# Optimization experiments

Hardware: AMD Instinct MI355X
Metric: run time of the kernel (lower is better)

The kernel has to match this reference:

```python
import jax, jax.numpy as jnp
import numpy as np

NEG_INF = -9e15
ALPHA = 0.2  # leaky relu slope


def setup_inputs() -> dict:
    key = jax.random.key(0)
    k1, k2, k3, k4 = jax.random.split(key, 4)
    B, N, Din = 8, 1024, 128
    H, D = 8, 16
    h = jax.random.normal(k1, (B, N, Din), dtype=jnp.float32)
    adj = jax.random.randint(k2, (B, N, N), 0, 2, dtype=jnp.int32)
    W = jax.random.normal(k3, (Din, H * D), dtype=jnp.float32) * 0.1
    a = jax.random.normal(k4, (H, 2 * D, 1), dtype=jnp.float32) * 0.1
    return {"h": h, "adj": adj, "W": W, "a": a}


def reference(h, adj, W, a):
    B, N, _ = h.shape
    H, twoD, _ = a.shape
    D = twoD // 2
    # Wh: [B, N, H, D]
    Wh = (h @ W).reshape(B, N, H, D)
    # Decompose additive attention: a . [Wh_i ; Wh_j] = a_src . Wh_i + a_dst . Wh_j
    a_src = a[:, :D, 0]   # [H, D]
    a_dst = a[:, D:, 0]   # [H, D]
    s_i = jnp.einsum('bnhd,hd->bhn', Wh, a_src)  # [B, H, N]
    s_j = jnp.einsum('bnhd,hd->bhn', Wh, a_dst)  # [B, H, N]
    scores = jax.nn.leaky_relu(s_i[:, :, :, None] + s_j[:, :, None, :], ALPHA)  # [B,H,N,N]
    scores = jnp.where(adj[:, None, :, :] == 0, NEG_INF, scores)
    attn = jax.nn.softmax(scores, axis=-1)  # [B, H, N, N]
    # Weighted aggregation over neighbors j
    h_prime = jnp.einsum('bhij,bjhd->bihd', attn, Wh).reshape(B, N, H * D)
    return h_prime
```

## Files before the change

kernel.cpp:

```cpp
#include <hip/hip_runtime.h>
#include <hip/hip_bf16.h>

constexpr int B   = 8;
constexpr int N   = 1024;
constexpr int DIN = 128;
constexpr int H   = 8;
constexpr int D   = 16;
constexpr int HD  = 128;
constexpr int TI  = 16;
constexpr int TJ  = 128;
constexpr int NT  = N / TJ;

#define LOG2E 1.4426950408889634f
#define TCLAMP 30.0f

typedef __attribute__((ext_vector_type(8))) short bf16x8;
typedef __attribute__((ext_vector_type(4))) float f32x4;

__device__ inline float fast_exp2(float x) {
#if __has_builtin(__builtin_amdgcn_exp2f)
    return __builtin_amdgcn_exp2f(x);
#else
    return exp2f(x);
#endif
}

__global__ __launch_bounds__(256) void k_proj(
    const float* __restrict__ hsrc,
    const float* __restrict__ W,
    const float* __restrict__ a,
    __hip_bfloat16* __restrict__ WhT,
    float* __restrict__ tI,
    float* __restrict__ tJ)
{
    const int blk  = blockIdx.x;
    const int row0 = blk * 64;
    const int b    = row0 >> 10;
    const int n0   = row0 & (N - 1);
    const int t    = threadIdx.x;
    const int lane = t & 63, wave = t >> 6;
    const int mn   = lane & 15, kg = lane >> 4;

    __shared__ __align__(16) __hip_bfloat16 hA[64][136];
    __shared__ __align__(16) __hip_bfloat16 Wt[128][136];

    {
        const float4* hf = reinterpret_cast<const float4*>(hsrc + (size_t)row0 * DIN);
        #pragma unroll
        for (int u = 0; u < 8; ++u) {
            const int idx = t + u * 256;
            const float4 v = hf[idx];
            const int r = idx >> 5, c4 = (idx & 31) * 4;
            __hip_bfloat162 p0, p1;
            p0.x = __float2bfloat16(v.x); p0.y = __float2bfloat16(v.y);
            p1.x = __float2bfloat16(v.z); p1.y = __float2bfloat16(v.w);
            *reinterpret_cast<__hip_bfloat162*>(&hA[r][c4])     = p0;
            *reinterpret_cast<__hip_bfloat162*>(&hA[r][c4 + 2]) = p1;
        }
    }
    {
        const float4* wf = reinterpret_cast<const float4*>(W);
        #pragma unroll
        for (int u = 0; u < 16; ++u) {
            const int idx = t + u * 256;
            const float4 v = wf[idx];
            const int k = idx >> 5, c0 = (idx & 31) * 4;
            Wt[c0][k]     = __float2bfloat16(v.x);
            Wt[c0 + 1][k] = __float2bfloat16(v.y);
            Wt[c0 + 2][k] = __float2bfloat16(v.z);
            Wt[c0 + 3][k] = __float2bfloat16(v.w);
        }
    }
    __syncthreads();

    const int lr0 = wave * 16;
    f32x4 acc[8];
    #pragma unroll
    for (int f = 0; f < 8; ++f) acc[f] = (f32x4){0.f, 0.f, 0.f, 0.f};

    #pragma unroll
    for (int kk = 0; kk < 4; ++kk) {
        const bf16x8 af = *reinterpret_cast<const bf16x8*>(
            &hA[lr0 + mn][kk * 32 + kg * 8]);
        #pragma unroll
        for (int f = 0; f < 8; ++f) {
            const bf16x8 bf = *reinterpret_cast<const bf16x8*>(
                &Wt[f * 16 + mn][kk * 32 + kg * 8]);
            acc[f] = __builtin_amdgcn_mfma_f32_16x16x32_bf16(af, bf, acc[f], 0, 0, 0);
        }
    }

    #pragma unroll
    for (int f = 0; f < 8; ++f) {
        const float as = a[f * 32 + mn];
        const float ad = a[f * 32 + 16 + mn];
        #pragma unroll
        for (int r = 0; r < 4; ++r) {
            const int n = n0 + lr0 + kg * 4 + r;
            WhT[((size_t)(b * HD + f * 16 + mn)) * N + n] = __float2bfloat16(acc[f][r]);
            float vi = acc[f][r] * as;
            float vj = acc[f][r] * ad;
            #pragma unroll
            for (int m = 1; m < 16; m <<= 1) {
                vi += __shfl_xor(vi, m);
                vj += __shfl_xor(vj, m);
            }
            if (mn == 0) {
                tI[((size_t)(b * H + f)) * N + n] = fminf(vi * LOG2E, TCLAMP);
                tJ[((size_t)(b * H + f)) * N + n] = fminf(vj * LOG2E, TCLAMP);
            }
        }
    }
}

__global__ __launch_bounds__(512, 4) void k_attn(
    const int*            __restrict__ adj,
    const __hip_bfloat16* __restrict__ WhT,
    const float*          __restrict__ tI,
    const float*          __restrict__ tJ,
    float*                __restrict__ out)
{
    const int b    = blockIdx.y;
    const int i0   = blockIdx.x * TI;
    const int t    = threadIdx.x;
    const int lane = t & 63, wave = t >> 6;
    const int mn   = lane & 15, kg = lane >> 4;
    const int jp   = lane;
    const int ig2  = wave;

    __shared__ __align__(16) __hip_bfloat16 pl[2][H][TI][136];

    float A[2][8];
    #pragma unroll
    for (int ii = 0; ii < 2; ++ii)
        #pragma unroll
        for (int h = 0; h < 8; ++h)
            A[ii][h] = tI[((size_t)(b * H + h)) * N + i0 + 2 * ig2 + ii];

    f32x4 accO = {0.f, 0.f, 0.f, 0.f};
    f32x4 accD = {0.f, 0.f, 0.f, 0.f};
    bf16x8 ones;
    #pragma unroll
    for (int e = 0; e < 8; ++e) ones[e] = (short)0x3F80;

    const __hip_bfloat16* wbase =
        WhT + ((size_t)(b * HD + wave * 16 + mn)) * N + kg * 8;
    const float* tjb = tJ + (size_t)b * H * N + 2 * jp;
    const int*   ab0 = adj + ((size_t)(b * N) + i0 + 2 * ig2) * N + 2 * jp;
    const int*   ab1 = ab0 + N;

    float2 tjc[8];
    int2   avc[2];
    #pragma unroll
    for (int h = 0; h < 8; ++h)
        tjc[h] = *reinterpret_cast<const float2*>(tjb + (size_t)h * N);
    avc[0] = *reinterpret_cast<const int2*>(ab0);
    avc[1] = *reinterpret_cast<const int2*>(ab1);

    #pragma unroll
    for (int jt = 0; jt < NT; ++jt) {
        const int j0 = jt * TJ, buf = jt & 1;

        float2 tjn[8];
        int2   avn[2];
        if (jt < NT - 1) {
            #pragma unroll
            for (int h = 0; h < 8; ++h)
                tjn[h] = *reinterpret_cast<const float2*>(
                    tjb + (size_t)h * N + (jt + 1) * TJ);
            avn[0] = *reinterpret_cast<const int2*>(ab0 + (jt + 1) * TJ);
            avn[1] = *reinterpret_cast<const int2*>(ab1 + (jt + 1) * TJ);
        }

        #pragma unroll
        for (int ii = 0; ii < 2; ++ii) {
            const int ir = 2 * ig2 + ii;
            const bool m0 = avc[ii].x != 0;
            const bool m1 = avc[ii].y != 0;
            #pragma unroll
            for (int h = 0; h < 8; ++h) {
                const float x0 = A[ii][h] + tjc[h].x;
                float a0 = fmaxf(x0, 0.2f * x0);
                a0 = m0 ? a0 : -1.0e30f;
                const float x1 = A[ii][h] + tjc[h].y;
                float a1 = fmaxf(x1, 0.2f * x1);
                a1 = m1 ? a1 : -1.0e30f;
                __hip_bfloat162 pp;
                pp.x = __float2bfloat16(fast_exp2(a0));
                pp.y = __float2bfloat16(fast_exp2(a1));
                *reinterpret_cast<__hip_bfloat162*>(&pl[buf][h][ir][2 * jp]) = pp;
            }
        }
        __syncthreads();

        #pragma unroll
        for (int kk = 0; kk < 4; ++kk) {
            const bf16x8 af = *reinterpret_cast<const bf16x8*>(
                &pl[buf][wave][mn][kk * 32 + kg * 8]);
            const bf16x8 bfr = *reinterpret_cast<const bf16x8*>(
                wbase + j0 + kk * 32);
            accO = __builtin_amdgcn_mfma_f32_16x16x32_bf16(af, bfr, accO, 0, 0, 0);
            accD = __builtin_amdgcn_mfma_f32_16x16x32_bf16(af, ones, accD, 0, 0, 0);
        }

        if (jt < NT - 1) {
            #pragma unroll
            for (int h = 0; h < 8; ++h) tjc[h] = tjn[h];
            avc[0] = avn[0];
            avc[1] = avn[1];
        }
    }

    #pragma unroll
    for (int r = 0; r < 4; ++r) {
        out[((size_t)(b * N) + i0 + kg * 4 + r) * HD + wave * 16 + mn] =
            accO[r] / accD[r];
    }
}

extern "C" void kernel_launch(void* const* d_in, const int* in_sizes, int n_in,
                              void* d_out, int out_size, void* d_ws, size_t ws_size,
                              hipStream_t stream)
{
    const float* h   = (const float*)d_in[0];
    const int*   adj = (const int*)d_in[1];
    const float* W   = (const float*)d_in[2];
    const float* a   = (const float*)d_in[3];
    float* out = (float*)d_out;

    float* ws = (float*)d_ws;
    float* tI = ws;
    float* tJ = ws + (size_t)B * H * N;
    __hip_bfloat16* WhT = (__hip_bfloat16*)(ws + (size_t)2 * B * H * N);

    k_proj<<<dim3(B * N / 64), dim3(256), 0, stream>>>(h, W, a, WhT, tI, tJ);
    k_attn<<<dim3(N / TI, B), dim3(512), 0, stream>>>(adj, WhT, tI, tJ, out);
}
```

Before: 47.65 us.

## Compute attention probabilities directly in MFMA register layout, drop LDS staging

The attention kernel now has each wave own one head and build the bf16 probability fragment for the MFMA A operand straight from global tJ and adj loads. This removes the shared-memory probability buffer and the per-tile __syncthreads. The trade-off is that each head's wave re-reads the adj row, so adj reads rise up to eightfold and rely on L2/cache hits, and the explicit register prefetch of the next tile is gone. The projection kernel also splits its work over 32-row blocks, with two waves per row tile each covering half the columns, which doubles the number of blocks.

```diff
diff --git a/kernel.cpp b/kernel.cpp
--- a/kernel.cpp
+++ b/kernel.cpp
@@ -33,29 +33,27 @@
     float* __restrict__ tI,
     float* __restrict__ tJ)
 {
-    const int blk  = blockIdx.x;
-    const int row0 = blk * 64;
+    const int row0 = blockIdx.x * 32;
     const int b    = row0 >> 10;
     const int n0   = row0 & (N - 1);
     const int t    = threadIdx.x;
     const int lane = t & 63, wave = t >> 6;
     const int mn   = lane & 15, kg = lane >> 4;
 
-    __shared__ __align__(16) __hip_bfloat16 hA[64][136];
+    __shared__ __align__(16) __hip_bfloat16 hA[32][136];
     __shared__ __align__(16) __hip_bfloat16 Wt[128][136];
 
     {
         const float4* hf = reinterpret_cast<const float4*>(hsrc + (size_t)row0 * DIN);
         #pragma unroll
-        for (int u = 0; u < 8; ++u) {
+        for (int u = 0; u < 4; ++u) {
             const int idx = t + u * 256;
             const float4 v = hf[idx];
             const int r = idx >> 5, c4 = (idx & 31) * 4;
-            __hip_bfloat162 p0, p1;
-            p0.x = __float2bfloat16(v.x); p0.y = __float2bfloat16(v.y);
-            p1.x = __float2bfloat16(v.z); p1.y = __float2bfloat16(v.w);
-            *reinterpret_cast<__hip_bfloat162*>(&hA[r][c4])     = p0;
-            *reinterpret_cast<__hip_bfloat162*>(&hA[r][c4 + 2]) = p1;
+            hA[r][c4]     = __float2bfloat16(v.x);
+            hA[r][c4 + 1] = __float2bfloat16(v.y);
+            hA[r][c4 + 2] = __float2bfloat16(v.z);
+            hA[r][c4 + 3] = __float2bfloat16(v.w);
         }
     }
     {
@@ -73,31 +71,34 @@
     }
     __syncthreads();
 
-    const int lr0 = wave * 16;
-    f32x4 acc[8];
+    const int lr0 = (wave >> 1) * 16;
+    const int ch  = wave & 1;
+    f32x4 acc[4];
     #pragma unroll
-    for (int f = 0; f < 8; ++f) acc[f] = (f32x4){0.f, 0.f, 0.f, 0.f};
+    for (int f = 0; f < 4; ++f) acc[f] = (f32x4){0.f, 0.f, 0.f, 0.f};
 
     #pragma unroll
     for (int kk = 0; kk < 4; ++kk) {
         const bf16x8 af = *reinterpret_cast<const bf16x8*>(
             &hA[lr0 + mn][kk * 32 + kg * 8]);
         #pragma unroll
-        for (int f = 0; f < 8; ++f) {
+        for (int f = 0; f < 4; ++f) {
             const bf16x8 bf = *reinterpret_cast<const bf16x8*>(
-                &Wt[f * 16 + mn][kk * 32 + kg * 8]);
+                &Wt[ch * 64 + f * 16 + mn][kk * 32 + kg * 8]);
             acc[f] = __builtin_amdgcn_mfma_f32_16x16x32_bf16(af, bf, acc[f], 0, 0, 0);
         }
     }
 
     #pragma unroll
-    for (int f = 0; f < 8; ++f) {
-        const float as = a[f * 32 + mn];
-        const float ad = a[f * 32 + 16 + mn];
+    for (int f = 0; f < 4; ++f) {
+        const int hh = ch * 4 + f;
+        const float as = a[hh * 32 + mn];
+        const float ad = a[hh * 32 + 16 + mn];
         #pragma unroll
         for (int r = 0; r < 4; ++r) {
             const int n = n0 + lr0 + kg * 4 + r;
-            WhT[((size_t)(b * HD + f * 16 + mn)) * N + n] = __float2bfloat16(acc[f][r]);
+            WhT[((size_t)(b * HD + ch * 64 + f * 16 + mn)) * N + n] =
+                __float2bfloat16(acc[f][r]);
             float vi = acc[f][r] * as;
             float vj = acc[f][r] * ad;
             #pragma unroll
@@ -106,8 +107,8 @@
                 vj += __shfl_xor(vj, m);
             }
             if (mn == 0) {
-                tI[((size_t)(b * H + f)) * N + n] = fminf(vi * LOG2E, TCLAMP);
-                tJ[((size_t)(b * H + f)) * N + n] = fminf(vj * LOG2E, TCLAMP);
+                tI[((size_t)(b * H + hh)) * N + n] = fminf(vi * LOG2E, TCLAMP);
+                tJ[((size_t)(b * H + hh)) * N + n] = fminf(vj * LOG2E, TCLAMP);
             }
         }
     }
@@ -123,19 +124,14 @@
     const int b    = blockIdx.y;
     const int i0   = blockIdx.x * TI;
     const int t    = threadIdx.x;
-    const int lane = t & 63, wave = t >> 6;
+    const int lane = t & 63, h = t >> 6;
     const int mn   = lane & 15, kg = lane >> 4;
-    const int jp   = lane;
-    const int ig2  = wave;
 
-    __shared__ __align__(16) __hip_bfloat16 pl[2][H][TI][136];
-
-    float A[2][8];
-    #pragma unroll
-    for (int ii = 0; ii < 2; ++ii)
-        #pragma unroll
-        for (int h = 0; h < 8; ++h)
-            A[ii][h] = tI[((size_t)(b * H + h)) * N + i0 + 2 * ig2 + ii];
+    const float Arow = tI[((size_t)(b * H + h)) * N + i0 + mn];
+    const float* tjrow = tJ + ((size_t)(b * H + h)) * N;
+    const int*   arow  = adj + ((size_t)(b * N) + i0 + mn) * N;
+    const __hip_bfloat16* wbase =
+        WhT + ((size_t)(b * HD + h * 16 + mn)) * N + kg * 8;
 
     f32x4 accO = {0.f, 0.f, 0.f, 0.f};
     f32x4 accD = {0.f, 0.f, 0.f, 0.f};
@@ -143,77 +139,37 @@
     #pragma unroll
     for (int e = 0; e < 8; ++e) ones[e] = (short)0x3F80;
 
-    const __hip_bfloat16* wbase =
-        WhT + ((size_t)(b * HD + wave * 16 + mn)) * N + kg * 8;
-    const float* tjb = tJ + (size_t)b * H * N + 2 * jp;
-    const int*   ab0 = adj + ((size_t)(b * N) + i0 + 2 * ig2) * N + 2 * jp;
-    const int*   ab1 = ab0 + N;
-
-    float2 tjc[8];
-    int2   avc[2];
-    #pragma unroll
-    for (int h = 0; h < 8; ++h)
-        tjc[h] = *reinterpret_cast<const float2*>(tjb + (size_t)h * N);
-    avc[0] = *reinterpret_cast<const int2*>(ab0);
-    avc[1] = *reinterpret_cast<const int2*>(ab1);
-
-    #pragma unroll
     for (int jt = 0; jt < NT; ++jt) {
-        const int j0 = jt * TJ, buf = jt & 1;
-
-        float2 tjn[8];
-        int2   avn[2];
-        if (jt < NT - 1) {
-            #pragma unroll
-            for (int h = 0; h < 8; ++h)
-                tjn[h] = *reinterpret_cast<const float2*>(
-                    tjb + (size_t)h * N + (jt + 1) * TJ);
-            avn[0] = *reinterpret_cast<const int2*>(ab0 + (jt + 1) * TJ);
-            avn[1] = *reinterpret_cast<const int2*>(ab1 + (jt + 1) * TJ);
-        }
-
-        #pragma unroll
-        for (int ii = 0; ii < 2; ++ii) {
-            const int ir = 2 * ig2 + ii;
-            const bool m0 = avc[ii].x != 0;
-            const bool m1 = avc[ii].y != 0;
-            #pragma unroll
-            for (int h = 0; h < 8; ++h) {
-                const float x0 = A[ii][h] + tjc[h].x;
-                float a0 = fmaxf(x0, 0.2f * x0);
-                a0 = m0 ? a0 : -1.0e30f;
-                const float x1 = A[ii][h] + tjc[h].y;
-                float a1 = fmaxf(x1, 0.2f * x1);
-                a1 = m1 ? a1 : -1.0e30f;
-                __hip_bfloat162 pp;
-                pp.x = __float2bfloat16(fast_exp2(a0));
-                pp.y = __float2bfloat16(fast_exp2(a1));
-                *reinterpret_cast<__hip_bfloat162*>(&pl[buf][h][ir][2 * jp]) = pp;
-            }
-        }
-        __syncthreads();
-
+        const int j0 = jt * TJ;
         #pragma unroll
         for (int kk = 0; kk < 4; ++kk) {
-            const bf16x8 af = *reinterpret_cast<const bf16x8*>(
-                &pl[buf][wave][mn][kk * 32 + kg * 8]);
+            const int jb = j0 + kk * 32 + kg * 8;
+            const float4 t0 = *reinterpret_cast<const float4*>(tjrow + jb);
+            const float4 t1 = *reinterpret_cast<const float4*>(tjrow + jb + 4);
+            const int4   a0 = *reinterpret_cast<const int4*>(arow + jb);
+            const int4   a1 = *reinterpret_cast<const int4*>(arow + jb + 4);
             const bf16x8 bfr = *reinterpret_cast<const bf16x8*>(
                 wbase + j0 + kk * 32);
+
+            const float tv[8] = {t0.x, t0.y, t0.z, t0.w, t1.x, t1.y, t1.z, t1.w};
+            const int   av[8] = {a0.x, a0.y, a0.z, a0.w, a1.x, a1.y, a1.z, a1.w};
+            bf16x8 af;
+            #pragma unroll
+            for (int e = 0; e < 8; ++e) {
+                const float x = Arow + tv[e];
+                float s = fmaxf(x, 0.2f * x);
+                s = (av[e] != 0) ? s : -1.0e30f;
+                const float p = fast_exp2(s);
+                af[e] = (short)__bfloat16_as_ushort(__float2bfloat16(p));
+            }
             accO = __builtin_amdgcn_mfma_f32_16x16x32_bf16(af, bfr, accO, 0, 0, 0);
             accD = __builtin_amdgcn_mfma_f32_16x16x32_bf16(af, ones, accD, 0, 0, 0);
-        }
-
-        if (jt < NT - 1) {
-            #pragma unroll
-            for (int h = 0; h < 8; ++h) tjc[h] = tjn[h];
-            avc[0] = avn[0];
-            avc[1] = avn[1];
         }
     }
 
     #pragma unroll
     for (int r = 0; r < 4; ++r) {
-        out[((size_t)(b * N) + i0 + kg * 4 + r) * HD + wave * 16 + mn] =
+        out[((size_t)(b * N) + i0 + kg * 4 + r) * HD + h * 16 + mn] =
             accO[r] / accD[r];
     }
 }
@@ -233,6 +189,6 @@
     float* tJ = ws + (size_t)B * H * N;
     __hip_bfloat16* WhT = (__hip_bfloat16*)(ws + (size_t)2 * B * H * N);
 
-    k_proj<<<dim3(B * N / 64), dim3(256), 0, stream>>>(h, W, a, WhT, tI, tJ);
+    k_proj<<<dim3(B * N / 32), dim3(256), 0, stream>>>(h, W, a, WhT, tI, tJ);
     k_attn<<<dim3(N / TI, B), dim3(512), 0, stream>>>(adj, WhT, tI, tJ, out);
 }
```

New measurement: 67.68 us. +42.0%, slower.
